# Optimization experiments

Hardware: AMD Instinct MI355X
Metric: run time of the kernel (lower is better)

## Reference

```python
import jax, jax.numpy as jnp
import numpy as np

N_SRC, N_MID, N_DST = 200000, 50000, 10000
D = 128
E1, E2 = 800000, 160000
EPS = 1e-12  # F.normalize eps


def setup_inputs() -> dict:
    key = jax.random.key(0)
    ks = jax.random.split(key, 12)
    s = 1.0 / np.sqrt(D)
    return {
        "x": jax.random.normal(ks[0], (N_SRC, D), jnp.float32),
        "W_l1": jax.random.uniform(ks[1], (D, D), jnp.float32, -s, s),
        "b_l1": jax.random.uniform(ks[2], (D,), jnp.float32, -s, s),
        "W_r1": jax.random.uniform(ks[3], (D, D), jnp.float32, -s, s),
        "W_l2": jax.random.uniform(ks[4], (D, D), jnp.float32, -s, s),
        "b_l2": jax.random.uniform(ks[5], (D,), jnp.float32, -s, s),
        "W_r2": jax.random.uniform(ks[6], (D, D), jnp.float32, -s, s),
        "row1": jax.random.randint(ks[7], (E1,), 0, N_SRC, jnp.int32),
        "col1": jax.random.randint(ks[8], (E1,), 0, N_MID, jnp.int32),
        "row2": jax.random.randint(ks[9], (E2,), 0, N_MID, jnp.int32),
        "col2": jax.random.randint(ks[10], (E2,), 0, N_DST, jnp.int32),
    }


def _sage_conv(x_src, x_dst, row, col, W_l, b_l, W_r, n_dst):
    # mean aggregation of source features over incoming edges (gather + scatter-add)
    msg = x_src[row]                                              # [E, D]
    agg = jax.ops.segment_sum(msg, col, num_segments=n_dst)       # [n_dst, D]
    deg = jax.ops.segment_sum(jnp.ones((row.shape[0],), x_src.dtype), col,
                              num_segments=n_dst)[:, None]        # [n_dst, 1]
    mean = jnp.where(deg > 0, agg / jnp.maximum(deg, 1.0), 0.0)
    out = mean @ W_l.T + b_l + x_dst @ W_r.T                      # lin_l + lin_r (root)
    # L2 normalize (normalize=True)
    norm = jnp.sqrt(jnp.sum(out * out, axis=-1, keepdims=True))
    return out / jnp.maximum(norm, EPS)


def reference(x, W_l1, b_l1, W_r1, W_l2, b_l2, W_r2, row1, col1, row2, col2):
    # layer 1: src = all sampled nodes, dst = first N_MID nodes
    h = _sage_conv(x, x[:N_MID], row1, col1, W_l1, b_l1, W_r1, N_MID)
    h = jax.nn.relu(h)  # dropout is identity in eval mode
    # layer 2: src = mid nodes, dst = first N_DST nodes (the batch targets)
    out = _sage_conv(h, h[:N_DST], row2, col2, W_l2, b_l2, W_r2, N_DST)
    return out
```

## Files before the change

### kernel.cpp

```cpp
#include <hip/hip_runtime.h>
#include <hip/hip_bf16.h>

#define DD 128
#define N_SRC 200000
#define N_MID 50000
#define N_DST 10000
#define E1 800000
#define E2 160000
#define CAP 48
#define CSTR 16

typedef unsigned short u16;
typedef unsigned int u32;
typedef __attribute__((ext_vector_type(8))) short s16x8;
typedef __attribute__((ext_vector_type(4))) float f32x4;
typedef __attribute__((ext_vector_type(4))) int i32x4;
typedef __attribute__((ext_vector_type(4))) float fv4;


__device__ __forceinline__ float bf_lo(u32 u) {
    union { u32 u; float f; } v; v.u = u << 16; return v.f;
}
__device__ __forceinline__ float bf_hi(u32 u) {
    union { u32 u; float f; } v; v.u = u & 0xffff0000u; return v.f;
}
__device__ __forceinline__ u32 f2bf_bits(float f) {
    union { float f; u32 u; } v; v.f = f;
    return (v.u + 0x7fffu + ((v.u >> 16) & 1u)) >> 16;
}
__device__ __forceinline__ u32 pack2bf(float lo, float hi) {
    return f2bf_bits(lo) | (f2bf_bits(hi) << 16);
}


#define FILL1_SLICE  4000
#define FILL1_BLOCKS 1600
#define FILL2_SLICE  4000
#define FILL2_BLOCKS 320
#define FILL_BLOCKS  (FILL1_BLOCKS + FILL2_BLOCKS)

#define NCONV8 (N_SRC * DD / 8)
#define WTF_T 8192
#define PREP_T (NCONV8 + WTF_T)
#define PREP_BLOCKS ((PREP_T + 255) / 256)
#define PF_BLOCKS (FILL_BLOCKS + PREP_BLOCKS)

__global__ __launch_bounds__(256, 8) void prep_fill(
    const float* __restrict__ x, u16* __restrict__ xb,
    const float* __restrict__ Wl1, const float* __restrict__ Wr1,
    u16* __restrict__ WTf1,
    const float* __restrict__ Wl2, const float* __restrict__ Wr2,
    u16* __restrict__ WTf2,
    const int* __restrict__ row1, const int* __restrict__ col1,
    const int* __restrict__ row2, const int* __restrict__ col2,
    int* __restrict__ cnt1, int* __restrict__ cnt2,
    int* __restrict__ csr1, int* __restrict__ csr2)
{
    const int b = blockIdx.x;
    const int tid = threadIdx.x;

    if (b < FILL_BLOCKS) {
        const int* __restrict__ rowp;
        const int* __restrict__ colp;
        int* __restrict__ cnt;
        int* __restrict__ csr;
        int e0, e1, div;
        const int shard = b & 7;
        if (b < FILL1_BLOCKS) {
            int slice = b >> 3;
            e0 = slice * FILL1_SLICE; e1 = e0 + FILL1_SLICE;
            rowp = row1; colp = col1; cnt = cnt1; csr = csr1; div = 6250;
        } else {
            int slice = (b - FILL1_BLOCKS) >> 3;
            e0 = slice * FILL2_SLICE; e1 = e0 + FILL2_SLICE;
            rowp = row2; colp = col2; cnt = cnt2; csr = csr2; div = 1250;
        }
        const int lo = shard * div;
        for (int base = e0 + tid * 4; base < e1; base += 1024) {
            i32x4 c4 = __builtin_nontemporal_load((const i32x4*)(colp + base));
            i32x4 r4 = __builtin_nontemporal_load((const i32x4*)(rowp + base));
            #pragma unroll
            for (int k = 0; k < 4; ++k) {
                int c = c4[k];
                if ((u32)(c - lo) < (u32)div) {
                    int p = atomicAdd(cnt + (size_t)c * CSTR, 1);
                    if (p < CAP) csr[c * CAP + p] = r4[k];
                }
            }
        }
    } else {
        int i = (b - FILL_BLOCKS) * 256 + tid;
        if (i < NCONV8) {
            const fv4* x4 = (const fv4*)x;
            fv4 a = __builtin_nontemporal_load(x4 + i * 2);
            fv4 bb = __builtin_nontemporal_load(x4 + i * 2 + 1);
            uint4 o;
            o.x = pack2bf(a[0], a[1]); o.y = pack2bf(a[2], a[3]);
            o.z = pack2bf(bb[0], bb[1]); o.w = pack2bf(bb[2], bb[3]);
            ((uint4*)xb)[i] = o;
        } else if (i < NCONV8 + WTF_T) {
            int t = i - NCONV8;
            int layer = t >> 12;
            int rem = t & 4095;
            int kt = rem >> 9;
            int nt = (rem >> 6) & 7;
            int lane = rem & 63;
            int gn = nt * 16 + (lane & 15);
            int k0 = kt * 32 + (lane >> 4) * 8;
            const float* Wl = layer ? Wl2 : Wl1;
            const float* Wr = layer ? Wr2 : Wr1;
            u16* WTf = layer ? WTf2 : WTf1;
            u32 o[4];
            #pragma unroll
            for (int p = 0; p < 4; ++p) {
                int ka = k0 + 2 * p, kb = ka + 1;
                float ea = (ka < 128) ? Wl[gn * 128 + ka] : Wr[gn * 128 + (ka - 128)];
                float eb = (kb < 128) ? Wl[gn * 128 + kb] : Wr[gn * 128 + (kb - 128)];
                o[p] = pack2bf(ea, eb);
            }
            ((uint4*)WTf)[(kt * 8 + nt) * 64 + lane] = make_uint4(o[0], o[1], o[2], o[3]);
        }
    }
}


template <int ROWS, bool RELU, int MINB>
__global__ __launch_bounds__(256, MINB) void sage_kernel(
    const u16* __restrict__ xsrc_b, const u16* __restrict__ xdst_b,
    const int* __restrict__ cnt, const int* __restrict__ csrf,
    const u16* __restrict__ WTf, const float* __restrict__ bias,
    float* __restrict__ out_f, u16* __restrict__ out_b,
    int n_dst, int fp32lim)
{
    __shared__ float smem[ROWS * 132];
    const int tid = threadIdx.x;
    const int i0 = blockIdx.x * ROWS;
    const int lane = tid & 63;
    const int w = tid >> 6;
    const int quarter = lane >> 4;
    const int l16 = lane & 15;
    const int half = lane >> 5;
    const int l32 = lane & 31;
    constexpr int RPW = ROWS / 4;

    const uint4* __restrict__ xs4 = (const uint4*)xsrc_b;
    const uint2* __restrict__ xd2 = (const uint2*)xdst_b;
    uint4* sA4 = (uint4*)smem;
    uint2* sA2 = (uint2*)smem;

    for (int q = 0; q < RPW; ++q) {
        int r = w * RPW + q;
        int i = i0 + r;
        if (i < n_dst) {
            int deg = cnt[(size_t)i * CSTR];
            if (deg > CAP) deg = CAP;
            float acc[8] = {0.f, 0.f, 0.f, 0.f, 0.f, 0.f, 0.f, 0.f};
            if (deg > 0) {
                const int* bp = csrf + (size_t)i * CAP;
                int iv = bp[lane < deg ? lane : deg - 1];
                for (int g = 0; g < deg; g += 16) {
                    #pragma unroll
                    for (int j = 0; j < 4; ++j) {
                        if (g + 4 * j < deg) {
                            int rel = g + 4 * j + quarter;
                            int idx = __shfl(iv, rel & 63);
                            float m = (rel < deg) ? 1.f : 0.f;
                            uint4 u = xs4[(size_t)idx * 16 + l16];
                            acc[0] += m * bf_lo(u.x); acc[1] += m * bf_hi(u.x);
                            acc[2] += m * bf_lo(u.y); acc[3] += m * bf_hi(u.y);
                            acc[4] += m * bf_lo(u.z); acc[5] += m * bf_hi(u.z);
                            acc[6] += m * bf_lo(u.w); acc[7] += m * bf_hi(u.w);
                        }
                    }
                }
                #pragma unroll
                for (int k = 0; k < 8; ++k) {
                    acc[k] += __shfl_xor(acc[k], 16);
                    acc[k] += __shfl_xor(acc[k], 32);
                }
            }
            float s = (deg > 0) ? 1.f / (float)deg : 0.f;
            if (quarter == 0) {
                uint4 o;
                o.x = pack2bf(acc[0] * s, acc[1] * s);
                o.y = pack2bf(acc[2] * s, acc[3] * s);
                o.z = pack2bf(acc[4] * s, acc[5] * s);
                o.w = pack2bf(acc[6] * s, acc[7] * s);
                sA4[r * 33 + l16] = o;
            }
            if (half == 1) {
                sA2[r * 66 + 32 + l32] = xd2[(size_t)i * 32 + l32];
            }
        } else {
            if (quarter == 0) sA4[r * 33 + l16] = make_uint4(0, 0, 0, 0);
            if (half == 1)    sA2[r * 66 + 32 + l32] = make_uint2(0, 0);
        }
    }
    __syncthreads();

    constexpr int MT = ROWS / 16;
    const int nt0 = w * 2;
    const s16x8* sAv = (const s16x8*)smem;
    const s16x8* Bv = (const s16x8*)WTf;

    f32x4 C[MT][2];
    #pragma unroll
    for (int mt = 0; mt < MT; ++mt)
        #pragma unroll
        for (int ni = 0; ni < 2; ++ni)
            C[mt][ni] = (f32x4){0.f, 0.f, 0.f, 0.f};

    #pragma unroll
    for (int kt = 0; kt < 8; ++kt) {
        s16x8 a[MT];
        #pragma unroll
        for (int mt = 0; mt < MT; ++mt)
            a[mt] = sAv[(mt * 16 + l16) * 33 + kt * 4 + quarter];
        s16x8 b0 = Bv[(kt * 8 + nt0) * 64 + lane];
        s16x8 b1 = Bv[(kt * 8 + nt0 + 1) * 64 + lane];
        #pragma unroll
        for (int mt = 0; mt < MT; ++mt) {
            C[mt][0] = __builtin_amdgcn_mfma_f32_16x16x32_bf16(a[mt], b0, C[mt][0], 0, 0, 0);
            C[mt][1] = __builtin_amdgcn_mfma_f32_16x16x32_bf16(a[mt], b1, C[mt][1], 0, 0, 0);
        }
    }

    __syncthreads();
    float* sOut = smem;

    #pragma unroll
    for (int ni = 0; ni < 2; ++ni) {
        int col = (nt0 + ni) * 16 + l16;
        float bc = bias[col];
        #pragma unroll
        for (int mt = 0; mt < MT; ++mt) {
            #pragma unroll
            for (int r = 0; r < 4; ++r) {
                int row = mt * 16 + quarter * 4 + r;
                sOut[row * 132 + col] = C[mt][ni][r] + bc;
            }
        }
    }
    __syncthreads();

    constexpr int R = ROWS / 8;
    const int ty = tid >> 5;
    const int tx = tid & 31;
    #pragma unroll
    for (int r = 0; r < R; ++r) {
        int row = ty * R + r;
        float4 v = *(const float4*)(&sOut[row * 132 + tx * 4]);
        float s = v.x * v.x + v.y * v.y + v.z * v.z + v.w * v.w;
        #pragma unroll
        for (int off = 1; off < 32; off <<= 1) s += __shfl_xor(s, off);
        float scale = 1.f / fmaxf(sqrtf(s), 1e-12f);
        float v0 = v.x * scale, v1 = v.y * scale, v2 = v.z * scale, v3 = v.w * scale;
        if (RELU) {
            v0 = fmaxf(v0, 0.f); v1 = fmaxf(v1, 0.f);
            v2 = fmaxf(v2, 0.f); v3 = fmaxf(v3, 0.f);
        }
        int i = i0 + row;
        if (i < n_dst) {
            if (i < fp32lim)
                *(float4*)(out_f + (size_t)i * DD + tx * 4) = make_float4(v0, v1, v2, v3);
            if (out_b) {
                uint2 ob;
                ob.x = pack2bf(v0, v1);
                ob.y = pack2bf(v2, v3);
                *(uint2*)(out_b + (size_t)i * DD + tx * 4) = ob;
            }
        }
    }
}


extern "C" void kernel_launch(void* const* d_in, const int* in_sizes, int n_in,
                              void* d_out, int out_size, void* d_ws, size_t ws_size,
                              hipStream_t stream) {
    const float* x    = (const float*)d_in[0];
    const float* Wl1  = (const float*)d_in[1];
    const float* bl1  = (const float*)d_in[2];
    const float* Wr1  = (const float*)d_in[3];
    const float* Wl2  = (const float*)d_in[4];
    const float* bl2  = (const float*)d_in[5];
    const float* Wr2  = (const float*)d_in[6];
    const int* row1   = (const int*)d_in[7];
    const int* col1   = (const int*)d_in[8];
    const int* row2   = (const int*)d_in[9];
    const int* col2   = (const int*)d_in[10];
    float* out = (float*)d_out;

    char* p = (char*)d_ws;
    u16* xb    = (u16*)p;   p += (size_t)N_SRC * DD * sizeof(u16);
    u16* hb    = (u16*)p;   p += (size_t)N_MID * DD * sizeof(u16);
    u16* WTf1  = (u16*)p;   p += (size_t)256 * 128 * sizeof(u16);
    u16* WTf2  = (u16*)p;   p += (size_t)256 * 128 * sizeof(u16);
    int* cnt1  = (int*)p;   p += (size_t)N_MID * CSTR * sizeof(int);
    int* cnt2  = (int*)p;   p += (size_t)N_DST * CSTR * sizeof(int);
    int* csr1  = (int*)p;   p += (size_t)N_MID * CAP * sizeof(int);
    int* csr2  = (int*)p;   p += (size_t)N_DST * CAP * sizeof(int);

    (void)hipMemsetAsync(cnt1, 0, (size_t)N_MID * CSTR * sizeof(int), stream);
    (void)hipMemsetAsync(cnt2, 0, (size_t)N_DST * CSTR * sizeof(int), stream);

    prep_fill<<<PF_BLOCKS, 256, 0, stream>>>(
        x, xb, Wl1, Wr1, WTf1, Wl2, Wr2, WTf2,
        row1, col1, row2, col2, cnt1, cnt2, csr1, csr2);

    sage_kernel<32, true, 6><<<(N_MID + 31) / 32, 256, 0, stream>>>(
        xb, xb, cnt1, csr1, WTf1, bl1, (float*)nullptr, hb, N_MID, 0);

    sage_kernel<16, false, 6><<<(N_DST + 15) / 16, 256, 0, stream>>>(
        hb, hb, cnt2, csr2, WTf2, bl2, out, (u16*)nullptr, N_DST, N_DST);
}
```

Measured before the change: 280.7 us.

## Fold layer-2 CSR fill into layer-1 kernel and prefetch neighbor indices

Moves the layer-2 edge bucketing out of the prep kernel into extra leading blocks of the layer-1 aggregation kernel, so it overlaps with layer-1 work. Degree counters are no longer padded to a 16-int stride, and a single memset now zeroes counters and CSR buffers together. The aggregation loop preloads per-row degrees into lanes and prefetches the next row's neighbor list. The merged memset clears more bytes than before, and denser counters may change atomic contention.

Result: faster. 273.3 us (-2.6%).

```diff
diff --git a/kernel.cpp b/kernel.cpp
--- a/kernel.cpp
+++ b/kernel.cpp
@@ -8,7 +8,6 @@
 #define E1 800000
 #define E2 160000
 #define CAP 48
-#define CSTR 16
 
 typedef unsigned short u16;
 typedef unsigned int u32;
@@ -35,15 +34,12 @@
 
 #define FILL1_SLICE  4000
 #define FILL1_BLOCKS 1600
-#define FILL2_SLICE  4000
-#define FILL2_BLOCKS 320
-#define FILL_BLOCKS  (FILL1_BLOCKS + FILL2_BLOCKS)
 
 #define NCONV8 (N_SRC * DD / 8)
 #define WTF_T 8192
 #define PREP_T (NCONV8 + WTF_T)
 #define PREP_BLOCKS ((PREP_T + 255) / 256)
-#define PF_BLOCKS (FILL_BLOCKS + PREP_BLOCKS)
+#define PF_BLOCKS (FILL1_BLOCKS + PREP_BLOCKS)
 
 __global__ __launch_bounds__(256, 8) void prep_fill(
     const float* __restrict__ x, u16* __restrict__ xb,
@@ -52,44 +48,29 @@
     const float* __restrict__ Wl2, const float* __restrict__ Wr2,
     u16* __restrict__ WTf2,
     const int* __restrict__ row1, const int* __restrict__ col1,
-    const int* __restrict__ row2, const int* __restrict__ col2,
-    int* __restrict__ cnt1, int* __restrict__ cnt2,
-    int* __restrict__ csr1, int* __restrict__ csr2)
+    int* __restrict__ cnt1, int* __restrict__ csr1)
 {
     const int b = blockIdx.x;
     const int tid = threadIdx.x;
 
-    if (b < FILL_BLOCKS) {
-        const int* __restrict__ rowp;
-        const int* __restrict__ colp;
-        int* __restrict__ cnt;
-        int* __restrict__ csr;
-        int e0, e1, div;
-        const int shard = b & 7;
-        if (b < FILL1_BLOCKS) {
-            int slice = b >> 3;
-            e0 = slice * FILL1_SLICE; e1 = e0 + FILL1_SLICE;
-            rowp = row1; colp = col1; cnt = cnt1; csr = csr1; div = 6250;
-        } else {
-            int slice = (b - FILL1_BLOCKS) >> 3;
-            e0 = slice * FILL2_SLICE; e1 = e0 + FILL2_SLICE;
-            rowp = row2; colp = col2; cnt = cnt2; csr = csr2; div = 1250;
-        }
-        const int lo = shard * div;
+    if (b < FILL1_BLOCKS) {
+        int slice = b >> 3, shard = b & 7;
+        int e0 = slice * FILL1_SLICE, e1 = e0 + FILL1_SLICE;
+        const int lo = shard * 6250;
         for (int base = e0 + tid * 4; base < e1; base += 1024) {
-            i32x4 c4 = __builtin_nontemporal_load((const i32x4*)(colp + base));
-            i32x4 r4 = __builtin_nontemporal_load((const i32x4*)(rowp + base));
+            i32x4 c4 = __builtin_nontemporal_load((const i32x4*)(col1 + base));
+            i32x4 r4 = __builtin_nontemporal_load((const i32x4*)(row1 + base));
             #pragma unroll
             for (int k = 0; k < 4; ++k) {
                 int c = c4[k];
-                if ((u32)(c - lo) < (u32)div) {
-                    int p = atomicAdd(cnt + (size_t)c * CSTR, 1);
-                    if (p < CAP) csr[c * CAP + p] = r4[k];
+                if ((u32)(c - lo) < 6250u) {
+                    int p = atomicAdd(cnt1 + c, 1);
+                    if (p < CAP) csr1[c * CAP + p] = r4[k];
                 }
             }
         }
     } else {
-        int i = (b - FILL_BLOCKS) * 256 + tid;
+        int i = (b - FILL1_BLOCKS) * 256 + tid;
         if (i < NCONV8) {
             const fv4* x4 = (const fv4*)x;
             fv4 a = __builtin_nontemporal_load(x4 + i * 2);
@@ -130,11 +111,34 @@
     const int* __restrict__ cnt, const int* __restrict__ csrf,
     const u16* __restrict__ WTf, const float* __restrict__ bias,
     float* __restrict__ out_f, u16* __restrict__ out_b,
-    int n_dst, int fp32lim)
+    int n_dst, int fp32lim,
+    const int* __restrict__ frow, const int* __restrict__ fcol,
+    int* __restrict__ fcnt, int* __restrict__ fcsr, int nfill)
 {
     __shared__ float smem[ROWS * 132];
     const int tid = threadIdx.x;
-    const int i0 = blockIdx.x * ROWS;
+
+    if (blockIdx.x < nfill) {
+        int bb = blockIdx.x;
+        int slice = bb >> 3, shard = bb & 7;
+        int e0 = slice * 4000, e1 = e0 + 4000;
+        const int lo = shard * 1250;
+        for (int base = e0 + tid * 4; base < e1; base += 1024) {
+            i32x4 c4 = __builtin_nontemporal_load((const i32x4*)(fcol + base));
+            i32x4 r4 = __builtin_nontemporal_load((const i32x4*)(frow + base));
+            #pragma unroll
+            for (int k = 0; k < 4; ++k) {
+                int c = c4[k];
+                if ((u32)(c - lo) < 1250u) {
+                    int p = atomicAdd(fcnt + c, 1);
+                    if (p < CAP) fcsr[c * CAP + p] = r4[k];
+                }
+            }
+        }
+        return;
+    }
+
+    const int i0 = (blockIdx.x - nfill) * ROWS;
     const int lane = tid & 63;
     const int w = tid >> 6;
     const int quarter = lane >> 4;
@@ -148,16 +152,30 @@
     uint4* sA4 = (uint4*)smem;
     uint2* sA2 = (uint2*)smem;
 
+    int degv = 0;
+    {
+        int rr = i0 + w * RPW + lane;
+        if (lane < RPW && rr < n_dst) degv = cnt[rr];
+    }
+    int iv_next = 0;
+    {
+        int i = i0 + w * RPW;
+        if (i < n_dst) iv_next = csrf[(size_t)i * CAP + lane];
+    }
+
     for (int q = 0; q < RPW; ++q) {
         int r = w * RPW + q;
         int i = i0 + r;
+        int deg = __shfl(degv, q);
+        if (deg > CAP) deg = CAP;
+        int iv = iv_next;
+        if (q + 1 < RPW) {
+            int i2 = i + 1;
+            iv_next = (i2 < n_dst) ? csrf[(size_t)i2 * CAP + lane] : 0;
+        }
         if (i < n_dst) {
-            int deg = cnt[(size_t)i * CSTR];
-            if (deg > CAP) deg = CAP;
             float acc[8] = {0.f, 0.f, 0.f, 0.f, 0.f, 0.f, 0.f, 0.f};
             if (deg > 0) {
-                const int* bp = csrf + (size_t)i * CAP;
-                int iv = bp[lane < deg ? lane : deg - 1];
                 for (int g = 0; g < deg; g += 16) {
                     #pragma unroll
                     for (int j = 0; j < 4; ++j) {
@@ -274,6 +292,8 @@
 }
 
 
+#define NF2 320
+
 extern "C" void kernel_launch(void* const* d_in, const int* in_sizes, int n_in,
                               void* d_out, int out_size, void* d_ws, size_t ws_size,
                               hipStream_t stream) {
@@ -295,21 +315,23 @@
     u16* hb    = (u16*)p;   p += (size_t)N_MID * DD * sizeof(u16);
     u16* WTf1  = (u16*)p;   p += (size_t)256 * 128 * sizeof(u16);
     u16* WTf2  = (u16*)p;   p += (size_t)256 * 128 * sizeof(u16);
-    int* cnt1  = (int*)p;   p += (size_t)N_MID * CSTR * sizeof(int);
-    int* cnt2  = (int*)p;   p += (size_t)N_DST * CSTR * sizeof(int);
+    char* zbase = p;
+    int* cnt1  = (int*)p;   p += (size_t)N_MID * sizeof(int);
+    int* cnt2  = (int*)p;   p += (size_t)N_DST * sizeof(int);
     int* csr1  = (int*)p;   p += (size_t)N_MID * CAP * sizeof(int);
     int* csr2  = (int*)p;   p += (size_t)N_DST * CAP * sizeof(int);
-
-    (void)hipMemsetAsync(cnt1, 0, (size_t)N_MID * CSTR * sizeof(int), stream);
-    (void)hipMemsetAsync(cnt2, 0, (size_t)N_DST * CSTR * sizeof(int), stream);
+    size_t zlen = (size_t)(p - zbase);
+
+    (void)hipMemsetAsync(zbase, 0, zlen, stream);
 
     prep_fill<<<PF_BLOCKS, 256, 0, stream>>>(
-        x, xb, Wl1, Wr1, WTf1, Wl2, Wr2, WTf2,
-        row1, col1, row2, col2, cnt1, cnt2, csr1, csr2);
-
-    sage_kernel<32, true, 6><<<(N_MID + 31) / 32, 256, 0, stream>>>(
-        xb, xb, cnt1, csr1, WTf1, bl1, (float*)nullptr, hb, N_MID, 0);
+        x, xb, Wl1, Wr1, WTf1, Wl2, Wr2, WTf2, row1, col1, cnt1, csr1);
+
+    sage_kernel<32, true, 6><<<NF2 + (N_MID + 31) / 32, 256, 0, stream>>>(
+        xb, xb, cnt1, csr1, WTf1, bl1, (float*)nullptr, hb, N_MID, 0,
+        row2, col2, cnt2, csr2, NF2);
 
     sage_kernel<16, false, 6><<<(N_DST + 15) / 16, 256, 0, stream>>>(
-        hb, hb, cnt2, csr2, WTf2, bl2, out, (u16*)nullptr, N_DST, N_DST);
-}
+        hb, hb, cnt2, csr2, WTf2, bl2, out, (u16*)nullptr, N_DST, N_DST,
+        nullptr, nullptr, nullptr, nullptr, 0);
+}
```
